# Performance work log

Measured on AMD Instinct MI355X. Metric: run time of the kernel, lower is better.

Reference implementation:

```python
import jax, jax.numpy as jnp
import numpy as np

B = 16384   # model_batches: parallel chaos-game chains
T = 512     # num_points: sequential IFS iterations per chain
N = 16      # num_matrices: affine functions in the IFS code


def setup_inputs() -> dict:
    key = jax.random.key(0)
    k1, k2, k3, k4, k5 = jax.random.split(key, 5)
    # uniform_sample1d(min=-5, max=5, dim=(B, 2))
    init_points = jax.random.uniform(k1, (B, 2), dtype=jnp.float32, minval=-5.0, maxval=5.0)
    # contractive affine maps: scale so spectral norm < 1 (ContractiveFunction)
    weights = jax.random.normal(k2, (N, 2, 2), dtype=jnp.float32) * 0.35
    biases = jax.random.normal(k3, (N, 2), dtype=jnp.float32) * 0.5
    opacities = jax.random.uniform(k4, (N,), dtype=jnp.float32)
    # fractal_code: precomputed per-step, per-chain function index (randomize_sequence=True)
    code = jax.random.randint(k5, (T, B), 0, N, dtype=jnp.int32)
    return {"init_points": init_points, "weights": weights, "biases": biases,
            "opacities": opacities, "code": code}


def reference(init_points, weights, biases, opacities, code):
    # ParallelIFS.forward: sequential chaos-game recurrence with gathered params.
    def step(p, idx):  # p: (B,2), idx: (B,) int
        W = weights[idx]            # (B,2,2) gather
        b = biases[idx]             # (B,2)
        p = jnp.einsum('bij,bj->bi', W, p) + b
        op = opacities[idx][:, None]  # (B,1)
        return p, jnp.concatenate([p, op], axis=1)  # emit (x, y, opacity)

    _, pts = jax.lax.scan(step, init_points, code)   # (T, B, 3)
    pts = pts.reshape(-1, 3)                          # (T*B, 3)
    ops = pts[:, 2:3]
    # apply_mv_transform: fixed model-view affine, world [-1,1] -> screen [0,1]
    tpoints = pts[:, :2] * 0.5 + 0.5
    top_points = jnp.concatenate([tpoints, ops], axis=1)
    return top_points
```

## Files before the change

### kernel.cpp

```cpp
#include <hip/hip_runtime.h>


#define B_PTS 16384
#define T_STEPS 512
#define N_TR 16
#define PTS_PER_BLK 64
#define WAVES 16
#define L_CHUNK 32
#define THREADS 1024
#define NPAIR 256

__global__ __launch_bounds__(THREADS, 1)
void ifs_scan_v2(const float* __restrict__ init_pts,
                 const float* __restrict__ weights,
                 const float* __restrict__ biases,
                 const float* __restrict__ opac,
                 const int*   __restrict__ code,
                 float*       __restrict__ out)
{
    __shared__ float4 tabA[N_TR];
    __shared__ float4 tabB[N_TR];
    __shared__ float4 pairA[NPAIR];
    __shared__ float2 pairB[NPAIR];
    __shared__ float4 mapsA[WAVES][PTS_PER_BLK];
    __shared__ float2 mapsB[WAVES][PTS_PER_BLK];

    const int tid  = threadIdx.x;
    const int lane = tid & 63;
    const int wv   = tid >> 6;
    const int base = blockIdx.x * PTS_PER_BLK;
    const int b    = base + lane;
    const int t0   = wv * L_CHUNK;

    int c[L_CHUNK];
    #pragma unroll
    for (int s = 0; s < L_CHUNK; ++s)
        c[s] = code[(size_t)(t0 + s) * B_PTS + b];

    if (tid < N_TR) {
        tabA[tid] = make_float4(weights[tid*4+0], weights[tid*4+1],
                                weights[tid*4+2], weights[tid*4+3]);
        tabB[tid] = make_float4(biases[tid*2+0], biases[tid*2+1], opac[tid], 0.f);
    }
    if (tid >= 64 && tid < 64 + NPAIR) {
        const int n = tid - 64;
        const int i = n & 15, j = n >> 4;
        const float ai = weights[i*4+0], bi = weights[i*4+1];
        const float ci = weights[i*4+2], di = weights[i*4+3];
        const float aj = weights[j*4+0], bj = weights[j*4+1];
        const float cj = weights[j*4+2], dj = weights[j*4+3];
        const float bxi = biases[i*2+0], byi = biases[i*2+1];
        const float bxj = biases[j*2+0], byj = biases[j*2+1];
        pairA[n] = make_float4(aj*ai + bj*ci, aj*bi + bj*di,
                               cj*ai + dj*ci, cj*bi + dj*di);
        pairB[n] = make_float2(aj*bxi + bj*byi + bxj,
                               cj*bxi + dj*byi + byj);
    }
    __syncthreads();

    float m00 = 1.f, m01 = 0.f, m10 = 0.f, m11 = 1.f, vx = 0.f, vy = 0.f;
    #pragma unroll
    for (int k = 0; k < L_CHUNK / 2; ++k) {
        const int pidx = (c[2*k+1] << 4) | c[2*k];
        const float4 P = pairA[pidx];
        const float2 V = pairB[pidx];
        const float n00 = P.x * m00 + P.y * m10;
        const float n01 = P.x * m01 + P.y * m11;
        const float n10 = P.z * m00 + P.w * m10;
        const float n11 = P.z * m01 + P.w * m11;
        const float nvx = P.x * vx + P.y * vy + V.x;
        const float nvy = P.z * vx + P.w * vy + V.y;
        m00 = n00; m01 = n01; m10 = n10; m11 = n11; vx = nvx; vy = nvy;
    }
    mapsA[wv][lane] = make_float4(m00, m01, m10, m11);
    mapsB[wv][lane] = make_float2(vx, vy);
    __syncthreads();

    const float2 p0 = *reinterpret_cast<const float2*>(&init_pts[(size_t)b * 2]);
    float px = p0.x, py = p0.y;
    for (int q = 0; q < wv; ++q) {
        const float4 M = mapsA[q][lane];
        const float2 V = mapsB[q][lane];
        const float nx = M.x * px + M.y * py + V.x;
        const float ny = M.z * px + M.w * py + V.y;
        px = nx; py = ny;
    }

    float* op = out + (size_t)((size_t)t0 * B_PTS + b) * 3;
    #pragma unroll 8
    for (int s = 0; s < L_CHUNK; ++s) {
        const int idx   = c[s];
        const float4 A  = tabA[idx];
        const float4 Bv = tabB[idx];
        const float nx = fmaf(A.x, px, fmaf(A.y, py, Bv.x));
        const float ny = fmaf(A.z, px, fmaf(A.w, py, Bv.y));
        px = nx; py = ny;
        op[0] = fmaf(px, 0.5f, 0.5f);
        op[1] = fmaf(py, 0.5f, 0.5f);
        op[2] = Bv.z;
        op += (size_t)B_PTS * 3;
    }
}

extern "C" void kernel_launch(void* const* d_in, const int* in_sizes, int n_in,
                              void* d_out, int out_size, void* d_ws, size_t ws_size,
                              hipStream_t stream) {
    const float* init_pts = (const float*)d_in[0];
    const float* weights  = (const float*)d_in[1];
    const float* biases   = (const float*)d_in[2];
    const float* opac     = (const float*)d_in[3];
    const int*   code     = (const int*)d_in[4];
    float*       out      = (float*)d_out;

    ifs_scan_v2<<<B_PTS / PTS_PER_BLK, THREADS, 0, stream>>>(
        init_pts, weights, biases, opac, code, out);
}
```

Measured before the change: 139.1 us.

## Pack code indices into nibbles and halve waves per block with longer chunks

Stores each chain's 64 per-step function indices as 4-bit nibbles in eight 32-bit registers instead of one int register per step. This lets each wave handle a 64-step chunk, so blocks shrink to 512 threads (8 waves) and the launch bound allows 4 blocks per CU for higher occupancy. Pair indices for the composed-map prefix come straight from byte extraction. The trade-off is a longer serial prefix chain per wave and extra shift and mask work to decode the indices.

```diff
diff --git a/kernel.cpp b/kernel.cpp
--- a/kernel.cpp
+++ b/kernel.cpp
@@ -5,13 +5,13 @@
 #define T_STEPS 512
 #define N_TR 16
 #define PTS_PER_BLK 64
-#define WAVES 16
-#define L_CHUNK 32
-#define THREADS 1024
+#define WAVES 8
+#define L_CHUNK 64
+#define THREADS 512
 #define NPAIR 256
 
-__global__ __launch_bounds__(THREADS, 1)
-void ifs_scan_v2(const float* __restrict__ init_pts,
+__global__ __launch_bounds__(THREADS, 4)
+void ifs_scan_v3(const float* __restrict__ init_pts,
                  const float* __restrict__ weights,
                  const float* __restrict__ biases,
                  const float* __restrict__ opac,
@@ -32,10 +32,15 @@
     const int b    = base + lane;
     const int t0   = wv * L_CHUNK;
 
-    int c[L_CHUNK];
+    unsigned nib[8];
     #pragma unroll
-    for (int s = 0; s < L_CHUNK; ++s)
-        c[s] = code[(size_t)(t0 + s) * B_PTS + b];
+    for (int j = 0; j < 8; ++j) {
+        unsigned acc = 0;
+        #pragma unroll
+        for (int k = 0; k < 8; ++k)
+            acc |= (unsigned)code[(size_t)(t0 + 8*j + k) * B_PTS + b] << (4*k);
+        nib[j] = acc;
+    }
 
     if (tid < N_TR) {
         tabA[tid] = make_float4(weights[tid*4+0], weights[tid*4+1],
@@ -60,17 +65,21 @@
 
     float m00 = 1.f, m01 = 0.f, m10 = 0.f, m11 = 1.f, vx = 0.f, vy = 0.f;
     #pragma unroll
-    for (int k = 0; k < L_CHUNK / 2; ++k) {
-        const int pidx = (c[2*k+1] << 4) | c[2*k];
-        const float4 P = pairA[pidx];
-        const float2 V = pairB[pidx];
-        const float n00 = P.x * m00 + P.y * m10;
-        const float n01 = P.x * m01 + P.y * m11;
-        const float n10 = P.z * m00 + P.w * m10;
-        const float n11 = P.z * m01 + P.w * m11;
-        const float nvx = P.x * vx + P.y * vy + V.x;
-        const float nvy = P.z * vx + P.w * vy + V.y;
-        m00 = n00; m01 = n01; m10 = n10; m11 = n11; vx = nvx; vy = nvy;
+    for (int j = 0; j < 8; ++j) {
+        const unsigned w = nib[j];
+        #pragma unroll
+        for (int kk = 0; kk < 4; ++kk) {
+            const int pidx = (w >> (8*kk)) & 255;
+            const float4 P = pairA[pidx];
+            const float2 V = pairB[pidx];
+            const float n00 = P.x * m00 + P.y * m10;
+            const float n01 = P.x * m01 + P.y * m11;
+            const float n10 = P.z * m00 + P.w * m10;
+            const float n11 = P.z * m01 + P.w * m11;
+            const float nvx = P.x * vx + P.y * vy + V.x;
+            const float nvy = P.z * vx + P.w * vy + V.y;
+            m00 = n00; m01 = n01; m10 = n10; m11 = n11; vx = nvx; vy = nvy;
+        }
     }
     mapsA[wv][lane] = make_float4(m00, m01, m10, m11);
     mapsB[wv][lane] = make_float2(vx, vy);
@@ -87,18 +96,22 @@
     }
 
     float* op = out + (size_t)((size_t)t0 * B_PTS + b) * 3;
-    #pragma unroll 8
-    for (int s = 0; s < L_CHUNK; ++s) {
-        const int idx   = c[s];
-        const float4 A  = tabA[idx];
-        const float4 Bv = tabB[idx];
-        const float nx = fmaf(A.x, px, fmaf(A.y, py, Bv.x));
-        const float ny = fmaf(A.z, px, fmaf(A.w, py, Bv.y));
-        px = nx; py = ny;
-        op[0] = fmaf(px, 0.5f, 0.5f);
-        op[1] = fmaf(py, 0.5f, 0.5f);
-        op[2] = Bv.z;
-        op += (size_t)B_PTS * 3;
+    #pragma unroll
+    for (int j = 0; j < 8; ++j) {
+        const unsigned w = nib[j];
+        #pragma unroll
+        for (int k = 0; k < 8; ++k) {
+            const int idx   = (w >> (4*k)) & 15;
+            const float4 A  = tabA[idx];
+            const float4 Bv = tabB[idx];
+            const float nx = fmaf(A.x, px, fmaf(A.y, py, Bv.x));
+            const float ny = fmaf(A.z, px, fmaf(A.w, py, Bv.y));
+            px = nx; py = ny;
+            op[0] = fmaf(px, 0.5f, 0.5f);
+            op[1] = fmaf(py, 0.5f, 0.5f);
+            op[2] = Bv.z;
+            op += (size_t)B_PTS * 3;
+        }
     }
 }
 
@@ -112,6 +125,6 @@
     const int*   code     = (const int*)d_in[4];
     float*       out      = (float*)d_out;
 
-    ifs_scan_v2<<<B_PTS / PTS_PER_BLK, THREADS, 0, stream>>>(
+    ifs_scan_v3<<<B_PTS / PTS_PER_BLK, THREADS, 0, stream>>>(
         init_pts, weights, biases, opac, code, out);
 }
```

Result: no change. 140.3 us (+0.9%).
